# Performance work log

Hardware: AMD Instinct MI355X
Metric: run time of the kernel (lower is better)

## Reference

```python
import jax, jax.numpy as jnp
import numpy as np

B, T, D, N, OUT = 1024, 128, 16, 64, 1
STD = 0.02


def setup_inputs() -> dict:
    key = jax.random.key(0)
    ks = jax.random.split(key, 17)
    r = lambda k, s: (jax.random.normal(k, s, dtype=jnp.float32) * STD)
    return {
        'x': jax.random.normal(ks[0], (B, T, D), dtype=jnp.float32),
        'U_j': r(ks[1], (D, 1, N)),
        'W_j': r(ks[2], (D, N, N)),
        'b_j': r(ks[3], (D, N)),
        'Wi_w': r(ks[4], (D * N, D * (N + 1))),
        'Wi_b': r(ks[5], (D * N,)),
        'Wf_w': r(ks[6], (D * N, D * (N + 1))),
        'Wf_b': r(ks[7], (D * N,)),
        'Wo_w': r(ks[8], (D * N, D * (N + 1))),
        'Wo_b': r(ks[9], (D * N,)),
        'F_alpha_n': r(ks[10], (D, N, 1)),
        'F_alpha_n_b': r(ks[11], (D, 1)),
        'F_beta_w': r(ks[12], (1, 2 * N)),
        'F_beta_b': r(ks[13], (1,)),
        'Phi_w': r(ks[14], (OUT, 2 * N)),
        'Phi_b': r(ks[15], (OUT,)),
    }


def reference(x, U_j, W_j, b_j, Wi_w, Wi_b, Wf_w, Wf_b, Wo_w, Wo_b,
              F_alpha_n, F_alpha_n_b, F_beta_w, F_beta_b, Phi_w, Phi_b):
    b = x.shape[0]
    d, n = W_j.shape[0], W_j.shape[1]
    u = U_j[:, 0, :]  # [d, n]

    def step(carry, x_t):  # x_t: [b, d]
        h, c = carry  # h: [b, d, n], c: [b, d*n]
        j = jnp.tanh(jnp.einsum('bdn,dnm->bdm', h, W_j)
                     + x_t[:, :, None] * u + b_j)
        inp = jnp.concatenate([x_t, h.reshape(b, -1)], axis=1)  # [b, d*(n+1)]
        i_t = jax.nn.sigmoid(inp @ Wi_w.T + Wi_b)
        f_t = jax.nn.sigmoid(inp @ Wf_w.T + Wf_b)
        o_t = jax.nn.sigmoid(inp @ Wo_w.T + Wo_b)
        c = c * f_t + i_t * j.reshape(b, -1)
        h = (o_t * jnp.tanh(c)).reshape(b, d, n)
        return (h, c), h

    h0 = jnp.zeros((b, d, n), dtype=x.dtype)
    c0 = jnp.zeros((b, d * n), dtype=x.dtype)
    (h_T, _), outs = jax.lax.scan(step, (h0, c0), jnp.swapaxes(x, 0, 1))
    outputs = jnp.transpose(outs, (1, 0, 2, 3))  # [b, t, d, n]

    # temporal attention per variable
    alphas = jnp.exp(jnp.tanh(
        jnp.einsum('btdn,dnk->btdk', outputs, F_alpha_n) + F_alpha_n_b))
    alphas = alphas / jnp.sum(alphas, axis=1, keepdims=True)
    g_n = jnp.sum(alphas * outputs, axis=1)  # [b, d, n]

    hg = jnp.concatenate([g_n, h_T], axis=2)  # [b, d, 2n]
    mu = hg @ Phi_w.T + Phi_b  # [b, d, out]
    betas = jnp.exp(jnp.tanh(hg @ F_beta_w.T + F_beta_b))  # [b, d, 1]
    betas = betas / jnp.sum(betas, axis=1, keepdims=True)
    return jnp.sum(betas * mu, axis=1)  # [b, out]
```

## Files before the change

### kernel.cpp

```cpp
#include <hip/hip_runtime.h>
#include <hip/hip_bf16.h>


namespace {
constexpr int B_  = 1024;
constexpr int T_  = 128;
constexpr int D_  = 16;
constexpr int DN_ = 1024;
constexpr int NIV = 8;

constexpr size_t INPBUF   = (size_t)128 * 1024 * 8 * 2;
constexpr size_t OFF_INP0 = 0;
constexpr size_t OFF_INP1 = INPBUF;
constexpr size_t OFF_FLAGS= 2 * INPBUF;
constexpr size_t OFF_SEH  = OFF_FLAGS + (size_t)16 * 128 * 4;
constexpr size_t OFF_SE   = OFF_SEH + (size_t)B_ * DN_ * 4;
constexpr size_t OFF_HT   = OFF_SE  + (size_t)B_ * D_ * 4;
constexpr size_t OFF_W2   = OFF_HT  + (size_t)B_ * DN_ * 4;
constexpr size_t OFF_WJ2  = OFF_W2  + (size_t)16 * 8 * 24576 * 2;
constexpr size_t OFF_WX2  = OFF_WJ2 + (size_t)16 * 4096 * 2;
constexpr size_t ZERO_BYTES = OFF_SEH;
}

typedef __attribute__((ext_vector_type(8))) __bf16 bf8;
typedef __attribute__((ext_vector_type(4))) float  f4;
typedef __attribute__((ext_vector_type(4))) unsigned int u32x4;

__device__ __forceinline__ unsigned short f2bf(float v) {
    unsigned int u = __float_as_uint(v);
    unsigned int r = u + 0x7FFFu + ((u >> 16) & 1u);
    return (unsigned short)(r >> 16);
}
__device__ __forceinline__ float rcpf(float x) { return __builtin_amdgcn_rcpf(x); }
__device__ __forceinline__ float tanhf_fast(float x) {
    x = fminf(fmaxf(x, -15.0f), 15.0f);
    float e = __expf(2.0f * x);
    return (e - 1.0f) * rcpf(e + 1.0f);
}
__device__ __forceinline__ float sigmoidf_fast(float x) {
    return rcpf(1.0f + __expf(-x));
}
__device__ __forceinline__ void gl16(const unsigned short* g, unsigned short* l) {
    __builtin_amdgcn_global_load_lds(
        (const __attribute__((address_space(1))) unsigned int*)g,
        (__attribute__((address_space(3))) unsigned int*)l, 16, 0, 0);
}
__device__ __forceinline__ void gl16c(const unsigned short* g, unsigned short* l) {
    __builtin_amdgcn_global_load_lds(
        (const __attribute__((address_space(1))) unsigned int*)g,
        (__attribute__((address_space(3))) unsigned int*)l, 16, 0, 17);
}
__device__ __forceinline__ void st16c(void* gaddr, u32x4 v) {
    unsigned long long a = (unsigned long long)gaddr;
    asm volatile("global_store_dwordx4 %0, %1, off sc0 sc1"
                 :: "v"(a), "v"(v) : "memory");
}
__device__ __forceinline__ void drain_vmem() {
    asm volatile("s_waitcnt vmcnt(0)" ::: "memory");
}

__global__ __launch_bounds__(256)
void prep_w2(const float* __restrict__ Wi, const float* __restrict__ Wf,
             const float* __restrict__ Wo, unsigned short* __restrict__ W2)
{
    int idx = blockIdx.x * 256 + threadIdx.x;
    if (idx >= 16 * 8 * 16 * 192 * 8) return;
    int e   = idx & 7;
    int t1  = idx >> 3;
    int col = t1 % 192;
    int t2  = t1 / 192;
    int kg  = t2 & 15;
    int t3  = t2 >> 4;
    int iv  = t3 & 7;
    int d   = t3 >> 3;
    int k   = 16 + iv * 128 + kg * 8 + e;
    int gate = col >> 6, c = col & 63;
    const float* W = (gate == 0) ? Wi : (gate == 1) ? Wf : Wo;
    W2[idx] = f2bf(W[(size_t)(d * 64 + c) * 1040 + k]);
}

__global__ __launch_bounds__(256)
void prep_misc(const float* __restrict__ Wj,
               const float* __restrict__ Wi, const float* __restrict__ Wf,
               const float* __restrict__ Wo,
               unsigned short* __restrict__ Wj2, unsigned short* __restrict__ Wx2)
{
    int idx = blockIdx.x * 256 + threadIdx.x;
    if (idx < 65536) {
        int e  = idx & 7;
        int m  = (idx >> 3) & 63;
        int kb = (idx >> 9) & 7;
        int d  = idx >> 12;
        int n  = kb * 8 + e;
        Wj2[idx] = f2bf(Wj[((size_t)d * 64 + n) * 64 + m]);
    } else if (idx < 65536 + 98304) {
        int i2  = idx - 65536;
        int e   = i2 & 7;
        int t1  = i2 >> 3;
        int col = t1 % 192;
        int t2  = t1 / 192;
        int kg  = t2 & 3;
        int d   = t2 >> 2;
        int k   = kg * 8 + e;
        int gate = col >> 6, c = col & 63;
        float v = 0.0f;
        if (k < 16) {
            const float* W = (gate == 0) ? Wi : (gate == 1) ? Wf : Wo;
            v = W[(size_t)(d * 64 + c) * 1040 + k];
        }
        Wx2[i2] = f2bf(v);
    }
}

__global__ __launch_bounds__(512, 1)
void scan_kernel(
    const float* __restrict__ x,
    const float* __restrict__ U_j, const float* __restrict__ b_j,
    const float* __restrict__ Wi_b, const float* __restrict__ Wf_b,
    const float* __restrict__ Wo_b,
    const float* __restrict__ F_an, const float* __restrict__ F_anb,
    const unsigned short* __restrict__ W2, const unsigned short* __restrict__ Wj2,
    const unsigned short* __restrict__ Wx2,
    unsigned short* __restrict__ inp0, unsigned short* __restrict__ inp1,
    int* __restrict__ flags,
    float* __restrict__ Seh, float* __restrict__ Se, float* __restrict__ hT)
{
    const int id  = blockIdx.x;
    const int d   = (id & 7) * 2 + ((id >> 3) & 1);
    const int bt  = id >> 4;
    const int b0  = bt * 64;
    const int tid = threadIdx.x;
    const int wv  = tid >> 6;
    const int cw  = wv & 3;
    const int rw  = wv >> 2;
    const int ln  = tid & 63;
    const int lr  = ln & 15;
    const int lg  = ln >> 4;
    const int coln  = cw * 16 + lr;
    const int rbase = rw * 32;

    __shared__ __align__(16) unsigned char smem[156416];
    unsigned short* a_sb0 = (unsigned short*)smem;
    unsigned short* a_sb1 = (unsigned short*)(smem + 16384);
    unsigned short* w_sb  = (unsigned short*)(smem + 32768);
    unsigned short* wj_s  = (unsigned short*)(smem + 131072);
    unsigned short* wx_s  = (unsigned short*)(smem + 139264);
    unsigned short* xa_s  = (unsigned short*)(smem + 151552);
    float* xd_s = (float*)(smem + 155648);
    float* fa_s = xd_s + 64;
    float* e_s  = xd_s + 128;
    typedef float (*hnrow_t)[66];
    hnrow_t hn_s = (hnrow_t)smem;

    const float uc   = U_j[d * 64 + coln];
    const float bc   = b_j[d * 64 + coln];
    const float bi_c = Wi_b[d * 64 + coln];
    const float bf_c = Wf_b[d * 64 + coln];
    const float bo_c = Wo_b[d * 64 + coln];
    const float fanb = F_anb[d];
    if (tid < 64) fa_s[tid] = F_an[d * 64 + tid];
    gl16(Wj2 + (size_t)d * 4096 + (size_t)(wv * 64 + ln) * 8, wj_s + wv * 512);
    #pragma unroll
    for (int i = 0; i < 2; ++i) {
        int g = wv + i * 8;
        if (g < 12)
            gl16(Wx2 + (size_t)d * 6144 + (size_t)(g * 64 + ln) * 8, wx_s + g * 512);
    }
    *(ushort4*)&xa_s[tid * 4] = make_ushort4(0, 0, 0, 0);
    const unsigned short* W2d = W2 + (size_t)d * (8 * 24576);
    const int jiv = d >> 1;
    const int jgb = (d & 1) * 8;

    float c_r[2][4]   = {};
    float seh_r[2][4] = {};
    float se_r = 0.0f;
    const f4 fz = {0.f, 0.f, 0.f, 0.f};

    for (int t = 0; t < T_; ++t) {
        const unsigned short* cur = (t & 1) ? inp1 : inp0;
        unsigned short*       nxt = (t & 1) ? inp0 : inp1;

        if (tid < 64) xd_s[tid] = x[(size_t)(b0 + tid) * 2048 + t * 16 + d];
        if (tid < 256) {
            int b = tid >> 2, q = tid & 3;
            float4 xv = *(const float4*)&x[(size_t)(b0 + b) * 2048 + t * 16 + q * 4];
            *(ushort4*)&xa_s[b * 32 + q * 4] =
                make_ushort4(f2bf(xv.x), f2bf(xv.y), f2bf(xv.z), f2bf(xv.w));
        }
        #pragma unroll
        for (int i = 0; i < 6; ++i) {
            int gw = wv * 6 + i;
            gl16(W2d + (size_t)(gw * 64 + ln) * 8, w_sb + gw * 512);
        }
        if (t > 0) {
            if (tid == 0) {
                while (__hip_atomic_load(&flags[bt * 128 + t], __ATOMIC_RELAXED,
                                         __HIP_MEMORY_SCOPE_AGENT) < 16)
                    __builtin_amdgcn_s_sleep(1);
            }
        }
        __syncthreads();

        #pragma unroll
        for (int i = 0; i < 2; ++i) {
            int ga = wv * 2 + i;
            gl16c(cur + ((size_t)ga * 1024 + b0 + ln) * 8, a_sb0 + ga * 512);
        }
        f4 acc[2][3];
        {
            bf8 wxg[3];
            #pragma unroll
            for (int g = 0; g < 3; ++g)
                wxg[g] = *(const bf8*)&wx_s[(lg * 192 + g * 64 + coln) * 8];
            #pragma unroll
            for (int mf = 0; mf < 2; ++mf) {
                bf8 xa = *(const bf8*)&xa_s[(rbase + mf * 16 + lr) * 32 + lg * 8];
                #pragma unroll
                for (int g = 0; g < 3; ++g)
                    acc[mf][g] = __builtin_amdgcn_mfma_f32_16x16x32_bf16(
                        xa, wxg[g], fz, 0, 0, 0);
            }
        }
        f4 jacc[2] = {fz, fz};
        __syncthreads();

        int buf = 0;
        for (int iv = 0; iv < NIV; ++iv) {
            unsigned short* a_cur = buf ? a_sb1 : a_sb0;
            if (iv < NIV - 1) {
                unsigned short* a_nxt = buf ? a_sb0 : a_sb1;
                #pragma unroll
                for (int i = 0; i < 2; ++i) {
                    int ga = wv * 2 + i;
                    gl16c(cur + ((size_t)((iv + 1) * 16 + ga) * 1024 + b0 + ln) * 8,
                          a_nxt + ga * 512);
                }
                const unsigned short* wsrc = W2d + (size_t)(iv + 1) * 24576;
                unsigned short* w_nxt = w_sb + (buf ^ 1) * 24576;
                #pragma unroll
                for (int i = 0; i < 6; ++i) {
                    int gw = wv * 6 + i;
                    gl16(wsrc + (size_t)(gw * 64 + ln) * 8, w_nxt + gw * 512);
                }
            }
            const unsigned short* w_cur = w_sb + buf * 24576;
            #pragma unroll
            for (int ks = 0; ks < 4; ++ks) {
                int kg = ks * 4 + lg;
                bf8 bwg[3];
                #pragma unroll
                for (int g = 0; g < 3; ++g)
                    bwg[g] = *(const bf8*)&w_cur[(kg * 192 + g * 64 + coln) * 8];
                #pragma unroll
                for (int mf = 0; mf < 2; ++mf) {
                    bf8 af = *(const bf8*)&a_cur[kg * 512 + (rbase + mf * 16 + lr) * 8];
                    #pragma unroll
                    for (int g = 0; g < 3; ++g)
                        acc[mf][g] = __builtin_amdgcn_mfma_f32_16x16x32_bf16(
                            af, bwg[g], acc[mf][g], 0, 0, 0);
                }
            }
            if (iv == jiv) {
                #pragma unroll
                for (int ks2 = 0; ks2 < 2; ++ks2) {
                    bf8 bw = *(const bf8*)&wj_s[((ks2 * 4 + lg) * 64 + coln) * 8];
                    #pragma unroll
                    for (int mf = 0; mf < 2; ++mf) {
                        bf8 ah = *(const bf8*)&a_cur[(jgb + ks2 * 4 + lg) * 512
                                                     + (rbase + mf * 16 + lr) * 8];
                        jacc[mf] = __builtin_amdgcn_mfma_f32_16x16x32_bf16(
                            ah, bw, jacc[mf], 0, 0, 0);
                    }
                }
            }
            __syncthreads();
            buf ^= 1;
        }

        float hn_r[2][4];
        #pragma unroll
        for (int mf = 0; mf < 2; ++mf) {
            #pragma unroll
            for (int r = 0; r < 4; ++r) {
                int row = rbase + mf * 16 + lg * 4 + r;
                float jr  = tanhf_fast(jacc[mf][r] + xd_s[row] * uc + bc);
                float iv_ = sigmoidf_fast(acc[mf][0][r] + bi_c);
                float fv  = sigmoidf_fast(acc[mf][1][r] + bf_c);
                float ov  = sigmoidf_fast(acc[mf][2][r] + bo_c);
                float cn  = c_r[mf][r] * fv + iv_ * jr;
                c_r[mf][r] = cn;
                float hn = ov * tanhf_fast(cn);
                hn_r[mf][r] = hn;
                hn_s[row][coln] = hn;
            }
        }
        __syncthreads();

        if (t < T_ - 1) {
            __align__(16) unsigned short pk[8];
            #pragma unroll
            for (int e = 0; e < 8; ++e) pk[e] = f2bf(hn_s[ln][wv * 8 + e]);
            st16c(nxt + ((size_t)(d * 8 + wv) * 1024 + b0 + ln) * 8,
                  *(const u32x4*)pk);
            drain_vmem();
            __syncthreads();
            if (tid == 0)
                atomicAdd(&flags[bt * 128 + (t + 1)], 1);
        }

        {
            int br_ = tid >> 3, q = tid & 7;
            float s = 0.0f;
            #pragma unroll
            for (int i2 = 0; i2 < 8; ++i2)
                s += hn_s[br_][q * 8 + i2] * fa_s[q * 8 + i2];
            s += __shfl_xor(s, 1);
            s += __shfl_xor(s, 2);
            s += __shfl_xor(s, 4);
            float e = __expf(tanhf_fast(s + fanb));
            if (q == 0) { e_s[br_] = e; se_r += e; }
        }
        __syncthreads();
        #pragma unroll
        for (int mf = 0; mf < 2; ++mf)
            #pragma unroll
            for (int r = 0; r < 4; ++r)
                seh_r[mf][r] += e_s[rbase + mf * 16 + lg * 4 + r] * hn_r[mf][r];
    }

    {
        int br_ = tid >> 3, q = tid & 7;
        #pragma unroll
        for (int i2 = 0; i2 < 2; ++i2) {
            float4 v;
            v.x = hn_s[br_][q * 8 + i2 * 4 + 0];
            v.y = hn_s[br_][q * 8 + i2 * 4 + 1];
            v.z = hn_s[br_][q * 8 + i2 * 4 + 2];
            v.w = hn_s[br_][q * 8 + i2 * 4 + 3];
            *(float4*)&hT[(size_t)(b0 + br_) * DN_ + d * 64 + q * 8 + i2 * 4] = v;
        }
        if (q == 0) Se[(size_t)(b0 + br_) * D_ + d] = se_r;
    }
    #pragma unroll
    for (int mf = 0; mf < 2; ++mf)
        #pragma unroll
        for (int r = 0; r < 4; ++r) {
            int row = rbase + mf * 16 + lg * 4 + r;
            Seh[((size_t)(b0 + row) * D_ + d) * 64 + coln] = seh_r[mf][r];
        }
}

__global__ __launch_bounds__(64)
void final_kernel(const float* __restrict__ hT,
                  const float* __restrict__ Se, const float* __restrict__ Seh,
                  const float* __restrict__ F_bw, const float* __restrict__ F_bb,
                  const float* __restrict__ Phi_w, const float* __restrict__ Phi_b,
                  float* __restrict__ out)
{
    int b = blockIdx.x;
    int tid = threadIdx.x;
    int d = tid >> 2, q = tid & 3;
    float se_inv = 1.0f / Se[(size_t)b * D_ + d];
    float mu = 0.0f, be = 0.0f;
    #pragma unroll
    for (int i = 0; i < 32; ++i) {
        int k = q * 32 + i;
        float hg = (k < 64) ? Seh[((size_t)b * D_ + d) * 64 + k] * se_inv
                            : hT[(size_t)b * DN_ + d * 64 + (k - 64)];
        mu += hg * Phi_w[k];
        be += hg * F_bw[k];
    }
    mu += __shfl_xor(mu, 1); mu += __shfl_xor(mu, 2);
    be += __shfl_xor(be, 1); be += __shfl_xor(be, 2);
    float mud = mu + Phi_b[0];
    float br  = __expf(tanhf_fast(be + F_bb[0]));
    float num = br * mud, den = br;
    #pragma unroll
    for (int off = 4; off < 64; off <<= 1) {
        num += __shfl_xor(num, off);
        den += __shfl_xor(den, off);
    }
    if (tid == 0) out[b] = num / den;
}

extern "C" void kernel_launch(void* const* d_in, const int* in_sizes, int n_in,
                              void* d_out, int out_size, void* d_ws, size_t ws_size,
                              hipStream_t stream)
{
    (void)in_sizes; (void)n_in; (void)out_size; (void)ws_size;
    const float* x     = (const float*)d_in[0];
    const float* U_j   = (const float*)d_in[1];
    const float* W_j   = (const float*)d_in[2];
    const float* b_j   = (const float*)d_in[3];
    const float* Wi_w  = (const float*)d_in[4];
    const float* Wi_b  = (const float*)d_in[5];
    const float* Wf_w  = (const float*)d_in[6];
    const float* Wf_b  = (const float*)d_in[7];
    const float* Wo_w  = (const float*)d_in[8];
    const float* Wo_b  = (const float*)d_in[9];
    const float* F_an  = (const float*)d_in[10];
    const float* F_anb = (const float*)d_in[11];
    const float* F_bw  = (const float*)d_in[12];
    const float* F_bb  = (const float*)d_in[13];
    const float* Phi_w = (const float*)d_in[14];
    const float* Phi_b = (const float*)d_in[15];
    float* out = (float*)d_out;

    char* ws = (char*)d_ws;
    unsigned short* inp0 = (unsigned short*)(ws + OFF_INP0);
    unsigned short* inp1 = (unsigned short*)(ws + OFF_INP1);
    int*   flags = (int*)(ws + OFF_FLAGS);
    float* Seh   = (float*)(ws + OFF_SEH);
    float* Se    = (float*)(ws + OFF_SE);
    float* hT    = (float*)(ws + OFF_HT);
    unsigned short* W2  = (unsigned short*)(ws + OFF_W2);
    unsigned short* Wj2 = (unsigned short*)(ws + OFF_WJ2);
    unsigned short* Wx2 = (unsigned short*)(ws + OFF_WX2);

    (void)hipMemsetAsync(d_ws, 0, ZERO_BYTES, stream);
    prep_w2<<<dim3(12288), dim3(256), 0, stream>>>(Wi_w, Wf_w, Wo_w, W2);
    prep_misc<<<dim3(640), dim3(256), 0, stream>>>(W_j, Wi_w, Wf_w, Wo_w, Wj2, Wx2);

    scan_kernel<<<dim3(256), dim3(512), 0, stream>>>(
        x, U_j, b_j, Wi_b, Wf_b, Wo_b, F_an, F_anb,
        W2, Wj2, Wx2, inp0, inp1, flags, Seh, Se, hT);

    final_kernel<<<dim3(B_), dim3(64), 0, stream>>>(hT, Se, Seh, F_bw, F_bb,
                                                    Phi_w, Phi_b, out);
}
```

Baseline: 1.370 ms.

## Replace syncthreads with partial vmcnt waits and raw barriers in recurrent loop

```diff
diff --git a/kernel.cpp b/kernel.cpp
--- a/kernel.cpp
+++ b/kernel.cpp
@@ -55,9 +55,15 @@
     asm volatile("global_store_dwordx4 %0, %1, off sc0 sc1"
                  :: "v"(a), "v"(v) : "memory");
 }
-__device__ __forceinline__ void drain_vmem() {
-    asm volatile("s_waitcnt vmcnt(0)" ::: "memory");
-}
+__device__ __forceinline__ void wait_vm(int n) {
+    if (n == 8)      asm volatile("s_waitcnt vmcnt(8)" ::: "memory");
+    else             asm volatile("s_waitcnt vmcnt(0)" ::: "memory");
+}
+__device__ __forceinline__ void lgk0() {
+    asm volatile("s_waitcnt lgkmcnt(0)" ::: "memory");
+}
+__device__ __forceinline__ void bar() { __builtin_amdgcn_s_barrier(); }
+__device__ __forceinline__ void sb0() { __builtin_amdgcn_sched_barrier(0); }
 
 __global__ __launch_bounds__(256)
 void prep_w2(const float* __restrict__ Wi, const float* __restrict__ Wf,
@@ -167,6 +173,7 @@
             gl16(Wx2 + (size_t)d * 6144 + (size_t)(g * 64 + ln) * 8, wx_s + g * 512);
     }
     *(ushort4*)&xa_s[tid * 4] = make_ushort4(0, 0, 0, 0);
+    wait_vm(0); lgk0(); bar();
     const unsigned short* W2d = W2 + (size_t)d * (8 * 24576);
     const int jiv = d >> 1;
     const int jgb = (d & 1) * 8;
@@ -199,7 +206,7 @@
                     __builtin_amdgcn_s_sleep(1);
             }
         }
-        __syncthreads();
+        lgk0(); bar(); sb0();
 
         #pragma unroll
         for (int i = 0; i < 2; ++i) {
@@ -222,13 +229,14 @@
             }
         }
         f4 jacc[2] = {fz, fz};
-        __syncthreads();
-
-        int buf = 0;
+
+        #pragma unroll
         for (int iv = 0; iv < NIV; ++iv) {
-            unsigned short* a_cur = buf ? a_sb1 : a_sb0;
+            const unsigned short* a_cur = (iv & 1) ? a_sb1 : a_sb0;
+            const unsigned short* w_cur = w_sb + (iv & 1) * 24576;
             if (iv < NIV - 1) {
-                unsigned short* a_nxt = buf ? a_sb0 : a_sb1;
+                unsigned short* a_nxt = (iv & 1) ? a_sb0 : a_sb1;
+                unsigned short* w_nxt = w_sb + ((iv & 1) ^ 1) * 24576;
                 #pragma unroll
                 for (int i = 0; i < 2; ++i) {
                     int ga = wv * 2 + i;
@@ -236,14 +244,17 @@
                           a_nxt + ga * 512);
                 }
                 const unsigned short* wsrc = W2d + (size_t)(iv + 1) * 24576;
-                unsigned short* w_nxt = w_sb + (buf ^ 1) * 24576;
                 #pragma unroll
                 for (int i = 0; i < 6; ++i) {
                     int gw = wv * 6 + i;
                     gl16(wsrc + (size_t)(gw * 64 + ln) * 8, w_nxt + gw * 512);
                 }
-            }
-            const unsigned short* w_cur = w_sb + buf * 24576;
+                wait_vm(8);
+            } else {
+                wait_vm(0);
+            }
+            sb0();
+            bar();
             #pragma unroll
             for (int ks = 0; ks < 4; ++ks) {
                 int kg = ks * 4 + lg;
@@ -273,8 +284,8 @@
                     }
                 }
             }
-            __syncthreads();
-            buf ^= 1;
+            lgk0();
+            bar();
         }
 
         float hn_r[2][4];
@@ -294,7 +305,7 @@
                 hn_s[row][coln] = hn;
             }
         }
-        __syncthreads();
+        lgk0(); bar();
 
         if (t < T_ - 1) {
             __align__(16) unsigned short pk[8];
@@ -302,8 +313,8 @@
             for (int e = 0; e < 8; ++e) pk[e] = f2bf(hn_s[ln][wv * 8 + e]);
             st16c(nxt + ((size_t)(d * 8 + wv) * 1024 + b0 + ln) * 8,
                   *(const u32x4*)pk);
-            drain_vmem();
-            __syncthreads();
+            wait_vm(0);
+            bar();
             if (tid == 0)
                 atomicAdd(&flags[bt * 128 + (t + 1)], 1);
         }
@@ -320,7 +331,7 @@
             float e = __expf(tanhf_fast(s + fanb));
             if (q == 0) { e_s[br_] = e; se_r += e; }
         }
-        __syncthreads();
+        lgk0(); bar();
         #pragma unroll
         for (int mf = 0; mf < 2; ++mf)
             #pragma unroll
```

After: 1.806 ms. +31.8%, slower.

## Replace per-step counter barrier with per-variable flags and rotated K-chunk order

Applied to the files above, without the earlier changes.

```diff
diff --git a/kernel.cpp b/kernel.cpp
--- a/kernel.cpp
+++ b/kernel.cpp
@@ -13,7 +13,8 @@
 constexpr size_t OFF_INP0 = 0;
 constexpr size_t OFF_INP1 = INPBUF;
 constexpr size_t OFF_FLAGS= 2 * INPBUF;
-constexpr size_t OFF_SEH  = OFF_FLAGS + (size_t)16 * 128 * 4;
+constexpr size_t FLAGSZ   = (size_t)16 * 128 * 16 * 4;
+constexpr size_t OFF_SEH  = OFF_FLAGS + FLAGSZ;
 constexpr size_t OFF_SE   = OFF_SEH + (size_t)B_ * DN_ * 4;
 constexpr size_t OFF_HT   = OFF_SE  + (size_t)B_ * D_ * 4;
 constexpr size_t OFF_W2   = OFF_HT  + (size_t)B_ * DN_ * 4;
@@ -48,7 +49,7 @@
 __device__ __forceinline__ void gl16c(const unsigned short* g, unsigned short* l) {
     __builtin_amdgcn_global_load_lds(
         (const __attribute__((address_space(1))) unsigned int*)g,
-        (__attribute__((address_space(3))) unsigned int*)l, 16, 0, 17);
+        (__attribute__((address_space(3))) unsigned int*)l, 16, 0, 19);
 }
 __device__ __forceinline__ void st16c(void* gaddr, u32x4 v) {
     unsigned long long a = (unsigned long long)gaddr;
@@ -57,6 +58,13 @@
 }
 __device__ __forceinline__ void drain_vmem() {
     asm volatile("s_waitcnt vmcnt(0)" ::: "memory");
+}
+__device__ __forceinline__ void wait_flag(const int* p) {
+    while (__hip_atomic_load(p, __ATOMIC_RELAXED, __HIP_MEMORY_SCOPE_AGENT) == 0)
+        __builtin_amdgcn_s_sleep(1);
+}
+__device__ __forceinline__ void post_flag(int* p) {
+    __hip_atomic_store(p, 1, __ATOMIC_RELAXED, __HIP_MEMORY_SCOPE_AGENT);
 }
 
 __global__ __launch_bounds__(256)
@@ -138,6 +146,8 @@
     const int lg  = ln >> 4;
     const int coln  = cw * 16 + lr;
     const int rbase = rw * 32;
+    const int siv0  = d >> 1;
+    const int jgb   = (d & 1) * 8;
 
     __shared__ __align__(16) unsigned char smem[156416];
     unsigned short* a_sb0 = (unsigned short*)smem;
@@ -168,8 +178,6 @@
     }
     *(ushort4*)&xa_s[tid * 4] = make_ushort4(0, 0, 0, 0);
     const unsigned short* W2d = W2 + (size_t)d * (8 * 24576);
-    const int jiv = d >> 1;
-    const int jgb = (d & 1) * 8;
 
     float c_r[2][4]   = {};
     float seh_r[2][4] = {};
@@ -179,6 +187,7 @@
     for (int t = 0; t < T_; ++t) {
         const unsigned short* cur = (t & 1) ? inp1 : inp0;
         unsigned short*       nxt = (t & 1) ? inp0 : inp1;
+        int* fD = flags + bt * 2048 + t * 16;
 
         if (tid < 64) xd_s[tid] = x[(size_t)(b0 + tid) * 2048 + t * 16 + d];
         if (tid < 256) {
@@ -187,24 +196,25 @@
             *(ushort4*)&xa_s[b * 32 + q * 4] =
                 make_ushort4(f2bf(xv.x), f2bf(xv.y), f2bf(xv.z), f2bf(xv.w));
         }
-        #pragma unroll
-        for (int i = 0; i < 6; ++i) {
-            int gw = wv * 6 + i;
-            gl16(W2d + (size_t)(gw * 64 + ln) * 8, w_sb + gw * 512);
+        {
+            const unsigned short* wsrc = W2d + (size_t)siv0 * 24576;
+            #pragma unroll
+            for (int i = 0; i < 6; ++i) {
+                int gw = wv * 6 + i;
+                gl16(wsrc + (size_t)(gw * 64 + ln) * 8, w_sb + gw * 512);
+            }
         }
         if (t > 0) {
-            if (tid == 0) {
-                while (__hip_atomic_load(&flags[bt * 128 + t], __ATOMIC_RELAXED,
-                                         __HIP_MEMORY_SCOPE_AGENT) < 16)
-                    __builtin_amdgcn_s_sleep(1);
-            }
+            wait_flag(fD + (d & ~1));
+            wait_flag(fD + (d | 1));
         }
         __syncthreads();
 
         #pragma unroll
         for (int i = 0; i < 2; ++i) {
             int ga = wv * 2 + i;
-            gl16c(cur + ((size_t)ga * 1024 + b0 + ln) * 8, a_sb0 + ga * 512);
+            gl16c(cur + ((size_t)(siv0 * 16 + ga) * 1024 + b0 + ln) * 8,
+                  a_sb0 + ga * 512);
         }
         f4 acc[2][3];
         {
@@ -225,25 +235,30 @@
         __syncthreads();
 
         int buf = 0;
-        for (int iv = 0; iv < NIV; ++iv) {
-            unsigned short* a_cur = buf ? a_sb1 : a_sb0;
-            if (iv < NIV - 1) {
+        for (int k = 0; k < NIV; ++k) {
+            const unsigned short* a_cur = buf ? a_sb1 : a_sb0;
+            const unsigned short* w_cur = w_sb + buf * 24576;
+            if (k < NIV - 1) {
+                int sivn = siv0 + k + 1; if (sivn >= NIV) sivn -= NIV;
+                if (t > 0) {
+                    wait_flag(fD + 2 * sivn);
+                    wait_flag(fD + 2 * sivn + 1);
+                }
                 unsigned short* a_nxt = buf ? a_sb0 : a_sb1;
+                unsigned short* w_nxt = w_sb + (buf ^ 1) * 24576;
                 #pragma unroll
                 for (int i = 0; i < 2; ++i) {
                     int ga = wv * 2 + i;
-                    gl16c(cur + ((size_t)((iv + 1) * 16 + ga) * 1024 + b0 + ln) * 8,
+                    gl16c(cur + ((size_t)(sivn * 16 + ga) * 1024 + b0 + ln) * 8,
                           a_nxt + ga * 512);
                 }
-                const unsigned short* wsrc = W2d + (size_t)(iv + 1) * 24576;
-                unsigned short* w_nxt = w_sb + (buf ^ 1) * 24576;
+                const unsigned short* wsrc = W2d + (size_t)sivn * 24576;
                 #pragma unroll
                 for (int i = 0; i < 6; ++i) {
                     int gw = wv * 6 + i;
                     gl16(wsrc + (size_t)(gw * 64 + ln) * 8, w_nxt + gw * 512);
                 }
             }
-            const unsigned short* w_cur = w_sb + buf * 24576;
             #pragma unroll
             for (int ks = 0; ks < 4; ++ks) {
                 int kg = ks * 4 + lg;
@@ -260,7 +275,7 @@
                             af, bwg[g], acc[mf][g], 0, 0, 0);
                 }
             }
-            if (iv == jiv) {
+            if (k == 0) {
                 #pragma unroll
                 for (int ks2 = 0; ks2 < 2; ++ks2) {
                     bf8 bw = *(const bf8*)&wj_s[((ks2 * 4 + lg) * 64 + coln) * 8];
@@ -305,7 +320,7 @@
             drain_vmem();
             __syncthreads();
             if (tid == 0)
-                atomicAdd(&flags[bt * 128 + (t + 1)], 1);
+                post_flag(flags + bt * 2048 + (t + 1) * 16 + d);
         }
 
         {
```

After: 1.991 ms. 1.45x slower.

## Switch scan kernel to 32x32x16 MFMA tiles with four waves per block

Applied to the files above, without the earlier changes.

```diff
diff --git a/kernel.cpp b/kernel.cpp
--- a/kernel.cpp
+++ b/kernel.cpp
@@ -22,9 +22,9 @@
 constexpr size_t ZERO_BYTES = OFF_SEH;
 }
 
-typedef __attribute__((ext_vector_type(8))) __bf16 bf8;
-typedef __attribute__((ext_vector_type(4))) float  f4;
-typedef __attribute__((ext_vector_type(4))) unsigned int u32x4;
+typedef __attribute__((ext_vector_type(8)))  __bf16 bf8;
+typedef __attribute__((ext_vector_type(16))) float  f16v;
+typedef __attribute__((ext_vector_type(4)))  unsigned int u32x4;
 
 __device__ __forceinline__ unsigned short f2bf(float v) {
     unsigned int u = __float_as_uint(v);
@@ -112,7 +112,7 @@
     }
 }
 
-__global__ __launch_bounds__(512, 1)
+__global__ __launch_bounds__(256, 1)
 void scan_kernel(
     const float* __restrict__ x,
     const float* __restrict__ U_j, const float* __restrict__ b_j,
@@ -131,13 +131,14 @@
     const int b0  = bt * 64;
     const int tid = threadIdx.x;
     const int wv  = tid >> 6;
-    const int cw  = wv & 3;
-    const int rw  = wv >> 2;
+    const int cw  = wv & 1;
+    const int rw  = wv >> 1;
     const int ln  = tid & 63;
-    const int lr  = ln & 15;
-    const int lg  = ln >> 4;
-    const int coln  = cw * 16 + lr;
+    const int lc  = ln & 31;
+    const int l5  = ln >> 5;
+    const int dnb   = cw * 32;
     const int rbase = rw * 32;
+    const int dn    = dnb + lc;
 
     __shared__ __align__(16) unsigned char smem[156416];
     unsigned short* a_sb0 = (unsigned short*)smem;
@@ -152,44 +153,51 @@
     typedef float (*hnrow_t)[66];
     hnrow_t hn_s = (hnrow_t)smem;
 
-    const float uc   = U_j[d * 64 + coln];
-    const float bc   = b_j[d * 64 + coln];
-    const float bi_c = Wi_b[d * 64 + coln];
-    const float bf_c = Wf_b[d * 64 + coln];
-    const float bo_c = Wo_b[d * 64 + coln];
+    const float uc   = U_j[d * 64 + dn];
+    const float bc   = b_j[d * 64 + dn];
+    const float bi_c = Wi_b[d * 64 + dn];
+    const float bf_c = Wf_b[d * 64 + dn];
+    const float bo_c = Wo_b[d * 64 + dn];
     const float fanb = F_anb[d];
     if (tid < 64) fa_s[tid] = F_an[d * 64 + tid];
-    gl16(Wj2 + (size_t)d * 4096 + (size_t)(wv * 64 + ln) * 8, wj_s + wv * 512);
     #pragma unroll
     for (int i = 0; i < 2; ++i) {
-        int g = wv + i * 8;
-        if (g < 12)
-            gl16(Wx2 + (size_t)d * 6144 + (size_t)(g * 64 + ln) * 8, wx_s + g * 512);
-    }
-    *(ushort4*)&xa_s[tid * 4] = make_ushort4(0, 0, 0, 0);
+        int g = wv * 2 + i;
+        gl16(Wj2 + (size_t)d * 4096 + (size_t)(g * 64 + ln) * 8, wj_s + g * 512);
+    }
+    #pragma unroll
+    for (int i = 0; i < 3; ++i) {
+        int g = wv * 3 + i;
+        gl16(Wx2 + (size_t)d * 6144 + (size_t)(g * 64 + ln) * 8, wx_s + g * 512);
+    }
+    {
+        *(ushort4*)&xa_s[tid * 8]     = make_ushort4(0, 0, 0, 0);
+        *(ushort4*)&xa_s[tid * 8 + 4] = make_ushort4(0, 0, 0, 0);
+    }
     const unsigned short* W2d = W2 + (size_t)d * (8 * 24576);
     const int jiv = d >> 1;
     const int jgb = (d & 1) * 8;
 
-    float c_r[2][4]   = {};
-    float seh_r[2][4] = {};
+    float c_r[16]   = {};
+    float seh_r[16] = {};
     float se_r = 0.0f;
-    const f4 fz = {0.f, 0.f, 0.f, 0.f};
+    const f16v fz16 = {0.f,0.f,0.f,0.f, 0.f,0.f,0.f,0.f,
+                       0.f,0.f,0.f,0.f, 0.f,0.f,0.f,0.f};
 
     for (int t = 0; t < T_; ++t) {
         const unsigned short* cur = (t & 1) ? inp1 : inp0;
         unsigned short*       nxt = (t & 1) ? inp0 : inp1;
 
         if (tid < 64) xd_s[tid] = x[(size_t)(b0 + tid) * 2048 + t * 16 + d];
-        if (tid < 256) {
+        {
             int b = tid >> 2, q = tid & 3;
             float4 xv = *(const float4*)&x[(size_t)(b0 + b) * 2048 + t * 16 + q * 4];
             *(ushort4*)&xa_s[b * 32 + q * 4] =
                 make_ushort4(f2bf(xv.x), f2bf(xv.y), f2bf(xv.z), f2bf(xv.w));
         }
         #pragma unroll
-        for (int i = 0; i < 6; ++i) {
-            int gw = wv * 6 + i;
+        for (int i = 0; i < 12; ++i) {
+            int gw = wv * 12 + i;
             gl16(W2d + (size_t)(gw * 64 + ln) * 8, w_sb + gw * 512);
         }
         if (t > 0) {
@@ -202,106 +210,92 @@
         __syncthreads();
 
         #pragma unroll
-        for (int i = 0; i < 2; ++i) {
-            int ga = wv * 2 + i;
+        for (int i = 0; i < 4; ++i) {
+            int ga = wv * 4 + i;
             gl16c(cur + ((size_t)ga * 1024 + b0 + ln) * 8, a_sb0 + ga * 512);
         }
-        f4 acc[2][3];
+        f16v acc[3];
         {
-            bf8 wxg[3];
+            bf8 xaf = *(const bf8*)&xa_s[(rbase + lc) * 32 + l5 * 8];
             #pragma unroll
-            for (int g = 0; g < 3; ++g)
-                wxg[g] = *(const bf8*)&wx_s[(lg * 192 + g * 64 + coln) * 8];
-            #pragma unroll
-            for (int mf = 0; mf < 2; ++mf) {
-                bf8 xa = *(const bf8*)&xa_s[(rbase + mf * 16 + lr) * 32 + lg * 8];
-                #pragma unroll
-                for (int g = 0; g < 3; ++g)
-                    acc[mf][g] = __builtin_amdgcn_mfma_f32_16x16x32_bf16(
-                        xa, wxg[g], fz, 0, 0, 0);
-            }
-        }
-        f4 jacc[2] = {fz, fz};
+            for (int g = 0; g < 3; ++g) {
+                bf8 wxf = *(const bf8*)&wx_s[((l5) * 192 + g * 64 + dnb + lc) * 8];
+                acc[g] = __builtin_amdgcn_mfma_f32_32x32x16_bf16(
+                    xaf, wxf, fz16, 0, 0, 0);
+            }
+        }
+        f16v jacc = fz16;
         __syncthreads();
 
         int buf = 0;
         for (int iv = 0; iv < NIV; ++iv) {
-            unsigned short* a_cur = buf ? a_sb1 : a_sb0;
+            const unsigned short* a_cur = buf ? a_sb1 : a_sb0;
+            const unsigned short* w_cur = w_sb + buf * 24576;
             if (iv < NIV - 1) {
                 unsigned short* a_nxt = buf ? a_sb0 : a_sb1;
+                unsigned short* w_nxt = w_sb + (buf ^ 1) * 24576;
                 #pragma unroll
-                for (int i = 0; i < 2; ++i) {
-                    int ga = wv * 2 + i;
+                for (int i = 0; i < 4; ++i) {
+                    int ga = wv * 4 + i;
                     gl16c(cur + ((size_t)((iv + 1) * 16 + ga) * 1024 + b0 + ln) * 8,
                           a_nxt + ga * 512);
                 }
                 const unsigned short* wsrc = W2d + (size_t)(iv + 1) * 24576;
-                unsigned short* w_nxt = w_sb + (buf ^ 1) * 24576;
                 #pragma unroll
-                for (int i = 0; i < 6; ++i) {
-                    int gw = wv * 6 + i;
+                for (int i = 0; i < 12; ++i) {
+                    int gw = wv * 12 + i;
                     gl16(wsrc + (size_t)(gw * 64 + ln) * 8, w_nxt + gw * 512);
                 }
             }
-            const unsigned short* w_cur = w_sb + buf * 24576;
             #pragma unroll
-            for (int ks = 0; ks < 4; ++ks) {
-                int kg = ks * 4 + lg;
-                bf8 bwg[3];
+            for (int ks = 0; ks < 8; ++ks) {
+                int koct = ks * 2 + l5;
+                bf8 af = *(const bf8*)&a_cur[koct * 512 + (rbase + lc) * 8];
                 #pragma unroll
-                for (int g = 0; g < 3; ++g)
-                    bwg[g] = *(const bf8*)&w_cur[(kg * 192 + g * 64 + coln) * 8];
-                #pragma unroll
-                for (int mf = 0; mf < 2; ++mf) {
-                    bf8 af = *(const bf8*)&a_cur[kg * 512 + (rbase + mf * 16 + lr) * 8];
-                    #pragma unroll
-                    for (int g = 0; g < 3; ++g)
-                        acc[mf][g] = __builtin_amdgcn_mfma_f32_16x16x32_bf16(
-                            af, bwg[g], acc[mf][g], 0, 0, 0);
+                for (int g = 0; g < 3; ++g) {
+                    bf8 bw = *(const bf8*)&w_cur[(koct * 192 + g * 64 + dnb + lc) * 8];
+                    acc[g] = __builtin_amdgcn_mfma_f32_32x32x16_bf16(
+                        af, bw, acc[g], 0, 0, 0);
                 }
             }
             if (iv == jiv) {
                 #pragma unroll
-                for (int ks2 = 0; ks2 < 2; ++ks2) {
-                    bf8 bw = *(const bf8*)&wj_s[((ks2 * 4 + lg) * 64 + coln) * 8];
-                    #pragma unroll
-                    for (int mf = 0; mf < 2; ++mf) {
-                        bf8 ah = *(const bf8*)&a_cur[(jgb + ks2 * 4 + lg) * 512
-                                                     + (rbase + mf * 16 + lr) * 8];
-                        jacc[mf] = __builtin_amdgcn_mfma_f32_16x16x32_bf16(
-                            ah, bw, jacc[mf], 0, 0, 0);
-                    }
+                for (int ks2 = 0; ks2 < 4; ++ks2) {
+                    bf8 ah = *(const bf8*)&a_cur[(jgb + ks2 * 2 + l5) * 512
+                                                 + (rbase + lc) * 8];
+                    bf8 bw = *(const bf8*)&wj_s[((ks2 * 2 + l5) * 64 + dnb + lc) * 8];
+                    jacc = __builtin_amdgcn_mfma_f32_32x32x16_bf16(
+                        ah, bw, jacc, 0, 0, 0);
                 }
             }
             __syncthreads();
             buf ^= 1;
         }
 
-        float hn_r[2][4];
         #pragma unroll
-        for (int mf = 0; mf < 2; ++mf) {
+        for (int r = 0; r < 16; ++r) {
+            int row = rbase + (r & 3) + 8 * (r >> 2) + 4 * l5;
+            float jr  = tanhf_fast(jacc[r] + xd_s[row] * uc + bc);
+            float iv_ = sigmoidf_fast(acc[0][r] + bi_c);
+            float fv  = sigmoidf_fast(acc[1][r] + bf_c);
+            float ov  = sigmoidf_fast(acc[2][r] + bo_c);
+            float cn  = c_r[r] * fv + iv_ * jr;
+            c_r[r] = cn;
+            float hn = ov * tanhf_fast(cn);
+            hn_s[row][dn] = hn;
+        }
+        __syncthreads();
+
+        if (t < T_ - 1) {
             #pragma unroll
-            for (int r = 0; r < 4; ++r) {
-                int row = rbase + mf * 16 + lg * 4 + r;
-                float jr  = tanhf_fast(jacc[mf][r] + xd_s[row] * uc + bc);
-                float iv_ = sigmoidf_fast(acc[mf][0][r] + bi_c);
-                float fv  = sigmoidf_fast(acc[mf][1][r] + bf_c);
-                float ov  = sigmoidf_fast(acc[mf][2][r] + bo_c);
-                float cn  = c_r[mf][r] * fv + iv_ * jr;
-                c_r[mf][r] = cn;
-                float hn = ov * tanhf_fast(cn);
-                hn_r[mf][r] = hn;
-                hn_s[row][coln] = hn;
-            }
-        }
-        __syncthreads();
-
-        if (t < T_ - 1) {
-            __align__(16) unsigned short pk[8];
-            #pragma unroll
-            for (int e = 0; e < 8; ++e) pk[e] = f2bf(hn_s[ln][wv * 8 + e]);
-            st16c(nxt + ((size_t)(d * 8 + wv) * 1024 + b0 + ln) * 8,
-                  *(const u32x4*)pk);
+            for (int i = 0; i < 2; ++i) {
+                int gw = wv * 2 + i;
+                __align__(16) unsigned short pk[8];
+                #pragma unroll
+                for (int e = 0; e < 8; ++e) pk[e] = f2bf(hn_s[ln][gw * 8 + e]);
+                st16c(nxt + ((size_t)(d * 8 + gw) * 1024 + b0 + ln) * 8,
+                      *(const u32x4*)pk);
+            }
             drain_vmem();
             __syncthreads();
             if (tid == 0)
@@ -309,45 +303,43 @@
         }
 
         {
-            int br_ = tid >> 3, q = tid & 7;
+            int b = tid >> 2, q = tid & 3;
             float s = 0.0f;
             #pragma unroll
-            for (int i2 = 0; i2 < 8; ++i2)
-                s += hn_s[br_][q * 8 + i2] * fa_s[q * 8 + i2];
+            for (int i2 = 0; i2 < 16; ++i2)
+                s += hn_s[b][q * 16 + i2] * fa_s[q * 16 + i2];
             s += __shfl_xor(s, 1);
             s += __shfl_xor(s, 2);
-            s += __shfl_xor(s, 4);
             float e = __expf(tanhf_fast(s + fanb));
-            if (q == 0) { e_s[br_] = e; se_r += e; }
+            if (q == 0) { e_s[b] = e; se_r += e; }
         }
         __syncthreads();
         #pragma unroll
-        for (int mf = 0; mf < 2; ++mf)
-            #pragma unroll
-            for (int r = 0; r < 4; ++r)
-                seh_r[mf][r] += e_s[rbase + mf * 16 + lg * 4 + r] * hn_r[mf][r];
+        for (int r = 0; r < 16; ++r) {
+            int row = rbase + (r & 3) + 8 * (r >> 2) + 4 * l5;
+            seh_r[r] += e_s[row] * hn_s[row][dn];
+        }
+        __syncthreads();
     }
 
     {
-        int br_ = tid >> 3, q = tid & 7;
+        int b = tid >> 2, q = tid & 3;
         #pragma unroll
-        for (int i2 = 0; i2 < 2; ++i2) {
+        for (int i2 = 0; i2 < 4; ++i2) {
             float4 v;
-            v.x = hn_s[br_][q * 8 + i2 * 4 + 0];
-            v.y = hn_s[br_][q * 8 + i2 * 4 + 1];
-            v.z = hn_s[br_][q * 8 + i2 * 4 + 2];
-            v.w = hn_s[br_][q * 8 + i2 * 4 + 3];
-            *(float4*)&hT[(size_t)(b0 + br_) * DN_ + d * 64 + q * 8 + i2 * 4] = v;
-        }
-        if (q == 0) Se[(size_t)(b0 + br_) * D_ + d] = se_r;
+            v.x = hn_s[b][q * 16 + i2 * 4 + 0];
+            v.y = hn_s[b][q * 16 + i2 * 4 + 1];
+            v.z = hn_s[b][q * 16 + i2 * 4 + 2];
+            v.w = hn_s[b][q * 16 + i2 * 4 + 3];
+            *(float4*)&hT[(size_t)(b0 + b) * DN_ + d * 64 + q * 16 + i2 * 4] = v;
+        }
+        if (q == 0) Se[(size_t)(b0 + b) * D_ + d] = se_r;
     }
     #pragma unroll
-    for (int mf = 0; mf < 2; ++mf)
-        #pragma unroll
-        for (int r = 0; r < 4; ++r) {
-            int row = rbase + mf * 16 + lg * 4 + r;
-            Seh[((size_t)(b0 + row) * D_ + d) * 64 + coln] = seh_r[mf][r];
-        }
+    for (int r = 0; r < 16; ++r) {
+        int row = rbase + (r & 3) + 8 * (r >> 2) + 4 * l5;
+        Seh[((size_t)(b0 + row) * D_ + d) * 64 + dn] = seh_r[r];
+    }
 }
 
 __global__ __launch_bounds__(64)
@@ -421,7 +413,7 @@
     prep_w2<<<dim3(12288), dim3(256), 0, stream>>>(Wi_w, Wf_w, Wo_w, W2);
     prep_misc<<<dim3(640), dim3(256), 0, stream>>>(W_j, Wi_w, Wf_w, Wo_w, Wj2, Wx2);
 
-    scan_kernel<<<dim3(256), dim3(512), 0, stream>>>(
+    scan_kernel<<<dim3(256), dim3(256), 0, stream>>>(
         x, U_j, b_j, Wi_b, Wf_b, Wo_b, F_an, F_anb,
         W2, Wj2, Wx2, inp0, inp1, flags, Seh, Se, hT);
 
```

Result: slower. 2.558 ms (+86.7%).
